# Optimization experiments

Hardware: AMD Instinct MI355X
Metric: run time of the kernel (lower is better)

Reference implementation:

```python
import jax, jax.numpy as jnp
import numpy as np

B, S, E, H = 1, 2048, 512, 8
D = E // H
N = B * S
WIN_HALF = 32  # attention_window 64 -> +/-32
ALPHA = 0.1
LN_EPS = 1e-12
NEG_INF = -1e9


def _build_window_edges():
    # windowed graph: dst i attends to src j with |i-j| <= WIN_HALF, within each batch block
    i = np.arange(S)
    offs = np.arange(-WIN_HALF, WIN_HALF + 1)
    src = i[:, None] + offs[None, :]
    dst = np.broadcast_to(i[:, None], src.shape)
    valid = (src >= 0) & (src < S)
    src, dst = src[valid], dst[valid]
    srcs, dsts = [], []
    for b in range(B):
        srcs.append(src + b * S)
        dsts.append(dst + b * S)
    return (np.concatenate(srcs).astype(np.int32),
            np.concatenate(dsts).astype(np.int32))


def setup_inputs() -> dict:
    key = jax.random.key(0)
    ks = jax.random.split(key, 12)
    sc = 1.0 / np.sqrt(E)
    src_np, dst_np = _build_window_edges()
    return {
        "hidden_states": jax.random.normal(ks[0], (B, S, E), dtype=jnp.float32),
        "attention_mask": jnp.zeros((B, S), dtype=jnp.float32),
        "edge_src": jnp.asarray(src_np),
        "edge_dst": jnp.asarray(dst_np),
        "Wq": jax.random.normal(ks[1], (E, E), dtype=jnp.float32) * sc,
        "bq": jnp.zeros((E,), dtype=jnp.float32),
        "Wk": jax.random.normal(ks[2], (E, E), dtype=jnp.float32) * sc,
        "bk": jnp.zeros((E,), dtype=jnp.float32),
        "Wv": jax.random.normal(ks[3], (E, E), dtype=jnp.float32) * sc,
        "bv": jnp.zeros((E,), dtype=jnp.float32),
        "Wo": jax.random.normal(ks[4], (E, E), dtype=jnp.float32) * sc,
        "bo": jnp.zeros((E,), dtype=jnp.float32),
        "ln_g": jnp.ones((E,), dtype=jnp.float32),
        "ln_b": jnp.zeros((E,), dtype=jnp.float32),
    }


def reference(hidden_states, attention_mask, edge_src, edge_dst,
              Wq, bq, Wk, bk, Wv, bv, Wo, bo, ln_g, ln_b):
    x = hidden_states  # (B,S,E); node ordering n = b*S + s (matches torch reshape)
    q = ((x @ Wq + bq) / jnp.sqrt(jnp.asarray(D, x.dtype))).reshape(N, H, D)
    k = (x @ Wk + bk).reshape(N, H, D)
    v = (x @ Wv + bv).reshape(N, H, D)

    mask = (attention_mask >= 0).reshape(N)  # bool per node

    # u_dot_v('k','q','score'): per-edge, per-head dot product
    score = jnp.einsum('ehd,ehd->eh', k[edge_src], q[edge_dst])  # (Eg,H)
    score = jnp.where(mask[edge_src][:, None], score, NEG_INF)

    # edge_softmax over incoming edges of each destination node
    smax = jax.ops.segment_max(score, edge_dst, num_segments=N)
    p = jnp.exp(score - smax[edge_dst])
    denom = jax.ops.segment_sum(p, edge_dst, num_segments=N)
    p = p / denom[edge_dst]  # (Eg,H)

    # 5 diffusion steps: h <- A h, blended with residual v (dropout off in eval)
    h = v
    for _ in range(5):
        m = h[edge_src] * p[:, :, None]                      # u_mul_e
        h = jax.ops.segment_sum(m, edge_dst, num_segments=N)  # sum('m','h')
        h = (1.0 - ALPHA) * h + ALPHA * v

    attn = h.reshape(B, S, E)

    # DiffuserSelfOutput: dense -> residual add -> LayerNorm
    y = attn @ Wo + bo + hidden_states
    mu = y.mean(-1, keepdims=True)
    var = ((y - mu) ** 2).mean(-1, keepdims=True)
    out = (y - mu) * jax.lax.rsqrt(var + LN_EPS) * ln_g + ln_b
    return out
```

## Files before the change

kernel.cpp:

```cpp
#include <hip/hip_runtime.h>
#include <math.h>

#define S_LEN 2048
#define E_DIM 512
#define NE (S_LEN * E_DIM)
#define H_NUM 8
#define WH 32
#define NOFF 65
#define PROW (H_NUM * NOFF)
#define PN (S_LEN * PROW)

typedef float f32x4 __attribute__((ext_vector_type(4)));
typedef short short8 __attribute__((ext_vector_type(8)));

__device__ __forceinline__ unsigned short f2bf(float f) {
    union { float f; unsigned u; } cv; cv.f = f;
    unsigned u = cv.u;
    u += 0x7fffu + ((u >> 16) & 1u);
    return (unsigned short)(u >> 16);
}
__device__ __forceinline__ unsigned pk2(float x, float y) {
    return (unsigned)f2bf(x) | ((unsigned)f2bf(y) << 16);
}

#define LGKM_BARRIER() do {                                   \
    __builtin_amdgcn_sched_barrier(0);                        \
    asm volatile("s_waitcnt lgkmcnt(0)" ::: "memory");        \
    __builtin_amdgcn_s_barrier();                             \
    __builtin_amdgcn_sched_barrier(0);                        \
} while (0)

__device__ __forceinline__ void mfma_gemm_f32(
    const float* __restrict__ A, const float* __restrict__ W,
    const float* __restrict__ bias, float* __restrict__ C,
    float scale, int m0, int n0)
{
    __shared__ unsigned short As[2][64 * 40];
    __shared__ unsigned short Bs[2][64 * 40];
    const int tid = threadIdx.x;
    const int lane = tid & 63, wave = tid >> 6;
    const int quad = lane >> 4, l16 = lane & 15;
    const int wr = (wave >> 1) * 32, wc = (wave & 1) * 32;
    const int ar = tid >> 2, ac = (tid & 3) * 8;
    const int bn = tid & 63, bk0 = (tid >> 6) * 8;

    f32x4 acc00 = {0.f,0.f,0.f,0.f}, acc01 = acc00, acc10 = acc00, acc11 = acc00;

    const float* Arow = A + (size_t)(m0 + ar) * E_DIM;

    float4 a0r[2], a1r[2];
    float  br[2][8];

#define QLOAD(s_, i_) do {                                                    \
        int kk_ = (i_) * 32;                                                  \
        a0r[s_] = *(const float4*)(Arow + kk_ + ac);                          \
        a1r[s_] = *(const float4*)(Arow + kk_ + ac + 4);                      \
        _Pragma("unroll")                                                     \
        for (int j_ = 0; j_ < 8; ++j_)                                        \
            br[s_][j_] = W[(size_t)(kk_ + bk0 + j_) * E_DIM + n0 + bn];       \
    } while (0)

#define QPACK(s_, b_) do {                                                    \
        uint4 ap_;                                                            \
        ap_.x = pk2(a0r[s_].x, a0r[s_].y); ap_.y = pk2(a0r[s_].z, a0r[s_].w); \
        ap_.z = pk2(a1r[s_].x, a1r[s_].y); ap_.w = pk2(a1r[s_].z, a1r[s_].w); \
        *(uint4*)(&As[b_][0] + ar * 40 + ac) = ap_;                           \
        uint4 bp_;                                                            \
        bp_.x = pk2(br[s_][0], br[s_][1]); bp_.y = pk2(br[s_][2], br[s_][3]); \
        bp_.z = pk2(br[s_][4], br[s_][5]); bp_.w = pk2(br[s_][6], br[s_][7]); \
        *(uint4*)(&Bs[b_][0] + bn * 40 + bk0) = bp_;                          \
    } while (0)

    QLOAD(0, 0);
    QPACK(0, 0);
    QLOAD(1, 1);
    LGKM_BARRIER();

#pragma unroll
    for (int it = 0; it < 16; ++it) {
        if (it < 14) QLOAD(it & 1, it + 2);

        const unsigned short* Ab = &As[it & 1][0];
        const unsigned short* Bb = &Bs[it & 1][0];
        short8 fa0 = *(const short8*)(Ab + (wr + l16) * 40 + quad * 8);
        short8 fa1 = *(const short8*)(Ab + (wr + 16 + l16) * 40 + quad * 8);
        short8 fb0 = *(const short8*)(Bb + (wc + l16) * 40 + quad * 8);
        short8 fb1 = *(const short8*)(Bb + (wc + 16 + l16) * 40 + quad * 8);
        acc00 = __builtin_amdgcn_mfma_f32_16x16x32_bf16(fa0, fb0, acc00, 0, 0, 0);
        acc01 = __builtin_amdgcn_mfma_f32_16x16x32_bf16(fa0, fb1, acc01, 0, 0, 0);
        acc10 = __builtin_amdgcn_mfma_f32_16x16x32_bf16(fa1, fb0, acc10, 0, 0, 0);
        acc11 = __builtin_amdgcn_mfma_f32_16x16x32_bf16(fa1, fb1, acc11, 0, 0, 0);

        if (it < 15) {
            QPACK((it + 1) & 1, (it + 1) & 1);
            LGKM_BARRIER();
        }
    }
#undef QLOAD
#undef QPACK

#pragma unroll
    for (int mi = 0; mi < 2; ++mi) {
#pragma unroll
        for (int ni = 0; ni < 2; ++ni) {
            f32x4 a = (mi == 0) ? ((ni == 0) ? acc00 : acc01)
                                : ((ni == 0) ? acc10 : acc11);
            int n = n0 + wc + ni * 16 + l16;
            float bval = bias[n];
#pragma unroll
            for (int r = 0; r < 4; ++r) {
                int m = m0 + wr + mi * 16 + quad * 4 + r;
                C[(size_t)m * E_DIM + n] = (a[r] + bval) * scale;
            }
        }
    }
}

__global__ __launch_bounds__(256)
void qkv_gemm(const float* __restrict__ x,
              const float* __restrict__ Wq, const float* __restrict__ bq,
              const float* __restrict__ Wk, const float* __restrict__ bk,
              const float* __restrict__ Wv, const float* __restrict__ bv,
              float* __restrict__ q, float* __restrict__ k, float* __restrict__ v)
{
    const float* W; const float* b; float* o; float sc;
    if (blockIdx.z == 0)      { W = Wq; b = bq; o = q; sc = 0.125f; }
    else if (blockIdx.z == 1) { W = Wk; b = bk; o = k; sc = 1.0f; }
    else                      { W = Wv; b = bv; o = v; sc = 1.0f; }
    mfma_gemm_f32(x, W, b, o, sc, blockIdx.y * 64, blockIdx.x * 64);
}

#define SDN 32
__global__ __launch_bounds__(256)
void scores_d1(const float* __restrict__ q, const float* __restrict__ k,
               const float* __restrict__ v, const float* __restrict__ amask,
               float* __restrict__ P, float* __restrict__ hA)
{
    const int i0 = blockIdx.x * SDN;
    const int h  = blockIdx.y;
    const int tid = threadIdx.x;
    __shared__ float ks[96 * 68];
    __shared__ float am[96];
    __shared__ float ps[SDN * NOFF];

    for (int e = tid; e < 96 * 16; e += 256) {
        int lr = e >> 4, c4 = e & 15;
        int j = i0 - WH + lr;
        int jc = min(max(j, 0), S_LEN - 1);
        *(float4*)(ks + lr * 68 + c4 * 4) =
            *(const float4*)(k + (size_t)jc * E_DIM + h * 64 + c4 * 4);
    }
    if (tid < 96) {
        int j = i0 - WH + tid;
        am[tid] = (j >= 0 && j < S_LEN) ? amask[j] : -1.0f;
    }

    const int dst = tid >> 3;
    const int og  = tid & 7;
    float4 qreg[16];
    {
        const float4* qrow = (const float4*)(q + (size_t)(i0 + dst) * E_DIM + h * 64);
#pragma unroll
        for (int t = 0; t < 16; ++t) qreg[t] = qrow[t];
    }
    __syncthreads();

    float sreg[9];
#pragma unroll
    for (int t = 0; t < 9; ++t) sreg[t] = -INFINITY;
#pragma unroll
    for (int t = 0; t < 9; ++t) {
        int off = og + 8 * t;
        if (off > 64) break;
        int j = i0 + dst + off - WH;
        if (j >= 0 && j < S_LEN) {
            int lr = dst + off;
            const float4* kr = (const float4*)(ks + lr * 68);
            float acc = 0.f;
#pragma unroll
            for (int u = 0; u < 16; ++u) {
                float4 a = qreg[u], bb = kr[u];
                acc += a.x * bb.x + a.y * bb.y + a.z * bb.z + a.w * bb.w;
            }
            sreg[t] = (am[lr] >= 0.f) ? acc : -1e9f;
        }
    }
    __syncthreads();

    for (int e = tid; e < 96 * 16; e += 256) {
        int lr = e >> 4, c4 = e & 15;
        int j = i0 - WH + lr;
        int jc = min(max(j, 0), S_LEN - 1);
        *(float4*)(ks + lr * 68 + c4 * 4) =
            *(const float4*)(v + (size_t)jc * E_DIM + h * 64 + c4 * 4);
    }

    float mx = sreg[0];
#pragma unroll
    for (int t = 1; t < 9; ++t) mx = fmaxf(mx, sreg[t]);
#pragma unroll
    for (int o = 1; o < 8; o <<= 1) mx = fmaxf(mx, __shfl_xor(mx, o, 64));
    float dn = 0.f;
#pragma unroll
    for (int t = 0; t < 9; ++t) {
        sreg[t] = expf(sreg[t] - mx);
        dn += sreg[t];
    }
#pragma unroll
    for (int o = 1; o < 8; o <<= 1) dn += __shfl_xor(dn, o, 64);
    float rinv = 1.f / dn;
#pragma unroll
    for (int t = 0; t < 9; ++t) {
        int off = og + 8 * t;
        if (off > 64) break;
        float pv = sreg[t] * rinv;
        P[(size_t)(i0 + dst) * PROW + h * NOFF + off] = pv;
        ps[dst * NOFF + off] = pv;
    }
    __syncthreads();

    {
        const int ci = tid & 15;
        const int ob = (tid >> 4) * 2;
        float4 a0 = {0,0,0,0}, a1 = a0;
        for (int lr = ob; lr < ob + 66; ++lr) {
            float4 hval = *(const float4*)(ks + lr * 68 + ci * 4);
            int o0 = lr - ob;
            if (o0 <= 64) {
                float p = ps[ob * NOFF + o0];
                a0.x += p * hval.x; a0.y += p * hval.y; a0.z += p * hval.z; a0.w += p * hval.w;
            }
            int o1 = o0 - 1;
            if ((unsigned)o1 <= 64u) {
                float p = ps[(ob + 1) * NOFF + o1];
                a1.x += p * hval.x; a1.y += p * hval.y; a1.z += p * hval.z; a1.w += p * hval.w;
            }
        }
#pragma unroll
        for (int r = 0; r < 2; ++r) {
            float4 a = r ? a1 : a0;
            float4 vv = *(const float4*)(ks + (WH + ob + r) * 68 + ci * 4);
            float4 o;
            o.x = 0.9f * a.x + 0.1f * vv.x;
            o.y = 0.9f * a.y + 0.1f * vv.y;
            o.z = 0.9f * a.z + 0.1f * vv.z;
            o.w = 0.9f * a.w + 0.1f * vv.w;
            *(float4*)(hA + (size_t)(i0 + ob + r) * E_DIM + h * 64 + ci * 4) = o;
        }
    }
}

__global__ __launch_bounds__(512)
void diffuse3m(const float* __restrict__ hin, const float* __restrict__ v,
               const float* __restrict__ P, float* __restrict__ hout)
{
    __shared__ unsigned short inT[64 * 264];
    __shared__ unsigned short m1T[64 * 200];
    __shared__ unsigned short ps[192 * 66];
    unsigned short* m2T = inT;
    const int i0 = blockIdx.x * 64;
    const int h  = blockIdx.y;
    const int c0 = h * 64;
    const int tid  = threadIdx.x;
    const int lane = tid & 63, wave = tid >> 6;
    const int quad = lane >> 4, l16 = lane & 15;

    for (int e = tid; e < 128 * 16; e += 512) {
        int rp = (e >> 4) * 2, c4 = (e & 15) * 4;
        int ja = min(max(i0 - 96 + rp,     0), S_LEN - 1);
        int jb = min(max(i0 - 96 + rp + 1, 0), S_LEN - 1);
        float4 ha = *(const float4*)(hin + (size_t)ja * E_DIM + c0 + c4);
        float4 hb = *(const float4*)(hin + (size_t)jb * E_DIM + c0 + c4);
        *(unsigned*)(inT + (c4 + 0) * 264 + rp) = pk2(ha.x, hb.x);
        *(unsigned*)(inT + (c4 + 1) * 264 + rp) = pk2(ha.y, hb.y);
        *(unsigned*)(inT + (c4 + 2) * 264 + rp) = pk2(ha.z, hb.z);
        *(unsigned*)(inT + (c4 + 3) * 264 + rp) = pk2(ha.w, hb.w);
    }
    for (int e = tid; e < 192 * 33; e += 512) {
        int mr = e / 33, t = e - mr * 33;
        int jc = min(max(i0 - 64 + mr, 0), S_LEN - 1);
        const float* pr = P + (size_t)jc * PROW + h * NOFF;
        if (t < 32)
            *(unsigned*)(ps + mr * 66 + t * 2) = pk2(pr[t * 2], pr[t * 2 + 1]);
        else
            ps[mr * 66 + 64] = f2bf(pr[64]);
    }
    __syncthreads();

#pragma unroll
    for (int uu = 0; uu < 3; ++uu) {
        int u = wave + uu * 8;
        int mtb = (u >> 1) * 16;
        int ntb = (u & 1) * 32;
        f32x4 a0 = {0.f,0.f,0.f,0.f}, a1 = a0;
        int ks0 = mtb >> 5;
        const int m = mtb + l16;
#pragma unroll
        for (int t = 0; t < 3; ++t) {
            int k0q = (ks0 + t) * 32 + quad * 8;
            short8 fa;
#pragma unroll
            for (int j = 0; j < 8; ++j) {
                int idx = k0q + j - m;
                int idc = min(max(idx, 0), 64);
                unsigned short pv = ps[m * 66 + idc];
                fa[j] = ((unsigned)idx <= 64u) ? (short)pv : (short)0;
            }
            short8 fb0 = *(const short8*)(inT + (ntb + l16) * 264 + k0q);
            short8 fb1 = *(const short8*)(inT + (ntb + 16 + l16) * 264 + k0q);
            a0 = __builtin_amdgcn_mfma_f32_16x16x32_bf16(fa, fb0, a0, 0, 0, 0);
            a1 = __builtin_amdgcn_mfma_f32_16x16x32_bf16(fa, fb1, a1, 0, 0, 0);
        }
#pragma unroll
        for (int nt = 0; nt < 2; ++nt) {
            f32x4 a = nt ? a1 : a0;
            int n = ntb + nt * 16 + l16;
            float o[4];
#pragma unroll
            for (int r = 0; r < 4; ++r) {
                int gm = min(max(i0 - 64 + mtb + quad * 4 + r, 0), S_LEN - 1);
                o[r] = 0.9f * a[r] + 0.1f * v[(size_t)gm * E_DIM + c0 + n];
            }
            *(unsigned*)(m1T + n * 200 + mtb + quad * 4)     = pk2(o[0], o[1]);
            *(unsigned*)(m1T + n * 200 + mtb + quad * 4 + 2) = pk2(o[2], o[3]);
        }
    }
    __syncthreads();

#pragma unroll
    for (int uu = 0; uu < 2; ++uu) {
        int u = wave + uu * 8;
        int mtb = (u >> 1) * 16;
        int ntb = (u & 1) * 32;
        f32x4 a0 = {0.f,0.f,0.f,0.f}, a1 = a0;
        int ks0 = mtb >> 5;
        const int m = mtb + l16;
#pragma unroll
        for (int t = 0; t < 3; ++t) {
            int k0q = (ks0 + t) * 32 + quad * 8;
            short8 fa;
#pragma unroll
            for (int j = 0; j < 8; ++j) {
                int idx = k0q + j - m;
                int idc = min(max(idx, 0), 64);
                unsigned short pv = ps[(m + 32) * 66 + idc];
                fa[j] = ((unsigned)idx <= 64u) ? (short)pv : (short)0;
            }
            short8 fb0 = *(const short8*)(m1T + (ntb + l16) * 200 + k0q);
            short8 fb1 = *(const short8*)(m1T + (ntb + 16 + l16) * 200 + k0q);
            a0 = __builtin_amdgcn_mfma_f32_16x16x32_bf16(fa, fb0, a0, 0, 0, 0);
            a1 = __builtin_amdgcn_mfma_f32_16x16x32_bf16(fa, fb1, a1, 0, 0, 0);
        }
        __syncthreads();
#pragma unroll
        for (int nt = 0; nt < 2; ++nt) {
            f32x4 a = nt ? a1 : a0;
            int n = ntb + nt * 16 + l16;
            float o[4];
#pragma unroll
            for (int r = 0; r < 4; ++r) {
                int gm = min(max(i0 - 32 + mtb + quad * 4 + r, 0), S_LEN - 1);
                o[r] = 0.9f * a[r] + 0.1f * v[(size_t)gm * E_DIM + c0 + n];
            }
            *(unsigned*)(m2T + n * 136 + mtb + quad * 4)     = pk2(o[0], o[1]);
            *(unsigned*)(m2T + n * 136 + mtb + quad * 4 + 2) = pk2(o[2], o[3]);
        }
    }
    __syncthreads();

    {
        int u = wave;
        int mtb = (u >> 1) * 16;
        int ntb = (u & 1) * 32;
        f32x4 a0 = {0.f,0.f,0.f,0.f}, a1 = a0;
        int ks0 = mtb >> 5;
        const int m = mtb + l16;
#pragma unroll
        for (int t = 0; t < 3; ++t) {
            int k0q = (ks0 + t) * 32 + quad * 8;
            short8 fa;
#pragma unroll
            for (int j = 0; j < 8; ++j) {
                int idx = k0q + j - m;
                int idc = min(max(idx, 0), 64);
                unsigned short pv = ps[(m + 64) * 66 + idc];
                fa[j] = ((unsigned)idx <= 64u) ? (short)pv : (short)0;
            }
            short8 fb0 = *(const short8*)(m2T + (ntb + l16) * 136 + k0q);
            short8 fb1 = *(const short8*)(m2T + (ntb + 16 + l16) * 136 + k0q);
            a0 = __builtin_amdgcn_mfma_f32_16x16x32_bf16(fa, fb0, a0, 0, 0, 0);
            a1 = __builtin_amdgcn_mfma_f32_16x16x32_bf16(fa, fb1, a1, 0, 0, 0);
        }
#pragma unroll
        for (int nt = 0; nt < 2; ++nt) {
            f32x4 a = nt ? a1 : a0;
            int n = ntb + nt * 16 + l16;
#pragma unroll
            for (int r = 0; r < 4; ++r) {
                int gm = i0 + mtb + quad * 4 + r;
                size_t base = (size_t)gm * E_DIM + c0 + n;
                hout[base] = 0.9f * a[r] + 0.1f * v[base];
            }
        }
    }
}

__global__ __launch_bounds__(512)
void oln4(const float* __restrict__ h4, const float* __restrict__ v,
          const float* __restrict__ P, const float* __restrict__ Wo,
          const float* __restrict__ bo, const float* __restrict__ x,
          const float* __restrict__ g, const float* __restrict__ lb,
          float* __restrict__ out)
{
    __shared__ unsigned short As16[16 * 520];
    __shared__ unsigned short Bs2[2][512 * 40];
    __shared__ float rsum[8][16], rsq[8][16];
    unsigned short* h4T  = &Bs2[0][0];
    unsigned short* ps16 = &Bs2[0][0] + 26624;

    const int tid = threadIdx.x;
    const int lane = tid & 63, wave = tid >> 6;
    const int quad = lane >> 4, l16 = lane & 15;
    const int m0 = blockIdx.x * 16;
    const int n = tid;

    for (int e = tid; e < 16 * 260; e += 512) {
        int mr = e / 260, t = e - mr * 260;
        const float* pr = P + (size_t)(m0 + mr) * PROW;
        *(unsigned*)(ps16 + mr * 528 + t * 2) = pk2(pr[t * 2], pr[t * 2 + 1]);
    }

    for (int hc = 0; hc < 2; ++hc) {
        for (int e = tid; e < 64 * 64; e += 512) {
            int r = e & 63, c4 = (e >> 6) * 4;
            int row = min(max(m0 - 32 + r, 0), S_LEN - 1);
            float4 hv = *(const float4*)(h4 + (size_t)row * E_DIM + hc * 256 + c4);
            h4T[(c4 + 0) * 104 + r] = f2bf(hv.x);
            h4T[(c4 + 1) * 104 + r] = f2bf(hv.y);
            h4T[(c4 + 2) * 104 + r] = f2bf(hv.z);
            h4T[(c4 + 3) * 104 + r] = f2bf(hv.w);
        }
        for (int e = tid; e < 32 * 64; e += 512) {
            int r = 64 + (e & 31), c4 = (e >> 5) * 4;
            int row = min(max(m0 - 32 + r, 0), S_LEN - 1);
            float4 hv = *(const float4*)(h4 + (size_t)row * E_DIM + hc * 256 + c4);
            h4T[(c4 + 0) * 104 + r] = f2bf(hv.x);
            h4T[(c4 + 1) * 104 + r] = f2bf(hv.y);
            h4T[(c4 + 2) * 104 + r] = f2bf(hv.z);
            h4T[(c4 + 3) * 104 + r] = f2bf(hv.w);
        }
        __syncthreads();

        {
            const int hd = hc * 4 + (wave >> 1);
            short8 fa[3];
#pragma unroll
            for (int t = 0; t < 3; ++t) {
                int k0q = t * 32 + quad * 8;
#pragma unroll
                for (int j = 0; j < 8; ++j) {
                    int idx = k0q + j - l16;
                    int idc = min(max(idx, 0), 64);
                    unsigned short pv = ps16[l16 * 528 + hd * NOFF + idc];
                    fa[t][j] = ((unsigned)idx <= 64u) ? (short)pv : (short)0;
                }
            }
#pragma unroll
            for (int nt = 0; nt < 2; ++nt) {
                int lc = wave * 32 + nt * 16;
                f32x4 ba = {0.f, 0.f, 0.f, 0.f};
#pragma unroll
                for (int t = 0; t < 3; ++t) {
                    short8 fb = *(const short8*)(h4T + (lc + l16) * 104 + t * 32 + quad * 8);
                    ba = __builtin_amdgcn_mfma_f32_16x16x32_bf16(fa[t], fb, ba, 0, 0, 0);
                }
                int gcol = hc * 256 + lc + l16;
#pragma unroll
                for (int r = 0; r < 4; ++r) {
                    int m = quad * 4 + r;
                    float vv = v[(size_t)(m0 + m) * E_DIM + gcol];
                    As16[m * 520 + gcol] = f2bf(0.9f * ba[r] + 0.1f * vv);
                }
            }
        }
        __syncthreads();
    }

    {
        float w0[32];
#pragma unroll
        for (int j = 0; j < 32; ++j)
            w0[j] = Wo[(size_t)j * E_DIM + n];
#pragma unroll
        for (int t = 0; t < 4; ++t) {
            uint4 bp;
            bp.x = pk2(w0[t*8+0], w0[t*8+1]); bp.y = pk2(w0[t*8+2], w0[t*8+3]);
            bp.z = pk2(w0[t*8+4], w0[t*8+5]); bp.w = pk2(w0[t*8+6], w0[t*8+7]);
            *(uint4*)(&Bs2[0][0] + n * 40 + t * 8) = bp;
        }
    }
    LGKM_BARRIER();

    f32x4 acc[4];
#pragma unroll
    for (int t = 0; t < 4; ++t) acc[t] = (f32x4){0.f,0.f,0.f,0.f};

#pragma unroll
    for (int it = 0; it < 16; ++it) {
        float wn[32];
        if (it < 15) {
#pragma unroll
            for (int j = 0; j < 32; ++j)
                wn[j] = Wo[(size_t)((it + 1) * 32 + j) * E_DIM + n];
        }

        short8 fa = *(const short8*)(As16 + l16 * 520 + it * 32 + quad * 8);
#pragma unroll
        for (int nt = 0; nt < 4; ++nt) {
            short8 fb = *(const short8*)(&Bs2[it & 1][0] +
                                         (wave * 64 + nt * 16 + l16) * 40 + quad * 8);
            acc[nt] = __builtin_amdgcn_mfma_f32_16x16x32_bf16(fa, fb, acc[nt], 0, 0, 0);
        }

        if (it < 15) {
#pragma unroll
            for (int t = 0; t < 4; ++t) {
                uint4 bp;
                bp.x = pk2(wn[t*8+0], wn[t*8+1]); bp.y = pk2(wn[t*8+2], wn[t*8+3]);
                bp.z = pk2(wn[t*8+4], wn[t*8+5]); bp.w = pk2(wn[t*8+6], wn[t*8+7]);
                *(uint4*)(&Bs2[(it + 1) & 1][0] + n * 40 + t * 8) = bp;
            }
            LGKM_BARRIER();
        }
    }

    float s[4] = {0.f,0.f,0.f,0.f}, s2[4] = {0.f,0.f,0.f,0.f};
#pragma unroll
    for (int nt = 0; nt < 4; ++nt) {
        int nc = wave * 64 + nt * 16 + l16;
        float bv = bo[nc];
#pragma unroll
        for (int r = 0; r < 4; ++r) {
            int m = m0 + quad * 4 + r;
            float vl = acc[nt][r] + bv + x[(size_t)m * E_DIM + nc];
            acc[nt][r] = vl;
            s[r] += vl; s2[r] += vl * vl;
        }
    }
#pragma unroll
    for (int o = 1; o < 16; o <<= 1) {
#pragma unroll
        for (int r = 0; r < 4; ++r) {
            s[r]  += __shfl_xor(s[r], o, 64);
            s2[r] += __shfl_xor(s2[r], o, 64);
        }
    }
    if (l16 == 0) {
#pragma unroll
        for (int r = 0; r < 4; ++r) {
            rsum[wave][quad * 4 + r] = s[r];
            rsq[wave][quad * 4 + r]  = s2[r];
        }
    }
    __syncthreads();
    float mu[4], rs[4];
#pragma unroll
    for (int r = 0; r < 4; ++r) {
        int rl = quad * 4 + r;
        float tot = 0.f, tot2 = 0.f;
#pragma unroll
        for (int w = 0; w < 8; ++w) { tot += rsum[w][rl]; tot2 += rsq[w][rl]; }
        float m_ = tot * (1.f / 512.f);
        float var = tot2 * (1.f / 512.f) - m_ * m_;
        mu[r] = m_; rs[r] = rsqrtf(var + 1e-12f);
    }
#pragma unroll
    for (int nt = 0; nt < 4; ++nt) {
        int nc = wave * 64 + nt * 16 + l16;
        float gv = g[nc], bbv = lb[nc];
#pragma unroll
        for (int r = 0; r < 4; ++r) {
            int m = m0 + quad * 4 + r;
            out[(size_t)m * E_DIM + nc] = (acc[nt][r] - mu[r]) * rs[r] * gv + bbv;
        }
    }
}

extern "C" void kernel_launch(void* const* d_in, const int* in_sizes, int n_in,
                              void* d_out, int out_size, void* d_ws, size_t ws_size,
                              hipStream_t stream)
{
    const float* x     = (const float*)d_in[0];
    const float* amask = (const float*)d_in[1];
    const float* Wq = (const float*)d_in[4];
    const float* bq = (const float*)d_in[5];
    const float* Wk = (const float*)d_in[6];
    const float* bk = (const float*)d_in[7];
    const float* Wv = (const float*)d_in[8];
    const float* bv = (const float*)d_in[9];
    const float* Wo = (const float*)d_in[10];
    const float* bo = (const float*)d_in[11];
    const float* lng = (const float*)d_in[12];
    const float* lnb = (const float*)d_in[13];
    float* out = (float*)d_out;

    float* ws = (float*)d_ws;
    float* q  = ws;
    float* k  = ws + (size_t)NE;
    float* v  = ws + (size_t)2 * NE;
    float* P  = ws + (size_t)3 * NE;
    float* hA = ws + (size_t)3 * NE + PN;
    float* hB = hA + (size_t)NE;

    qkv_gemm<<<dim3(8, 32, 3), 256, 0, stream>>>(x, Wq, bq, Wk, bk, Wv, bv, q, k, v);

    scores_d1<<<dim3(64, 8), 256, 0, stream>>>(q, k, v, amask, P, hA);

    diffuse3m<<<dim3(32, 8), 512, 0, stream>>>(hA, v, P, hB);

    oln4<<<128, 512, 0, stream>>>(hB, v, P, Wo, bo, x, lng, lnb, out);
}
```

Baseline: 165.3 us.

## Move fifth diffusion step into diffuse kernel and pass bf16 result to output GEMM

New measurement: 164.4 us. About the same (-0.6%).

```diff
diff --git a/kernel.cpp b/kernel.cpp
--- a/kernel.cpp
+++ b/kernel.cpp
@@ -251,13 +251,14 @@
 }
 
 __global__ __launch_bounds__(512)
-void diffuse3m(const float* __restrict__ hin, const float* __restrict__ v,
-               const float* __restrict__ P, float* __restrict__ hout)
+void diffuse4m(const float* __restrict__ hin, const float* __restrict__ v,
+               const float* __restrict__ P, unsigned short* __restrict__ h5b)
 {
-    __shared__ unsigned short inT[64 * 264];
-    __shared__ unsigned short m1T[64 * 200];
-    __shared__ unsigned short ps[192 * 66];
+    __shared__ unsigned short inT[64 * 328];
+    __shared__ unsigned short m1T[64 * 264];
+    __shared__ unsigned short ps[256 * 66];
     unsigned short* m2T = inT;
+    unsigned short* m3T = m1T;
     const int i0 = blockIdx.x * 64;
     const int h  = blockIdx.y;
     const int c0 = h * 64;
@@ -265,25 +266,65 @@
     const int lane = tid & 63, wave = tid >> 6;
     const int quad = lane >> 4, l16 = lane & 15;
 
-    for (int e = tid; e < 128 * 16; e += 512) {
+    for (int e = tid; e < 160 * 16; e += 512) {
         int rp = (e >> 4) * 2, c4 = (e & 15) * 4;
-        int ja = min(max(i0 - 96 + rp,     0), S_LEN - 1);
-        int jb = min(max(i0 - 96 + rp + 1, 0), S_LEN - 1);
+        int ja = min(max(i0 - 128 + rp,     0), S_LEN - 1);
+        int jb = min(max(i0 - 128 + rp + 1, 0), S_LEN - 1);
         float4 ha = *(const float4*)(hin + (size_t)ja * E_DIM + c0 + c4);
         float4 hb = *(const float4*)(hin + (size_t)jb * E_DIM + c0 + c4);
-        *(unsigned*)(inT + (c4 + 0) * 264 + rp) = pk2(ha.x, hb.x);
-        *(unsigned*)(inT + (c4 + 1) * 264 + rp) = pk2(ha.y, hb.y);
-        *(unsigned*)(inT + (c4 + 2) * 264 + rp) = pk2(ha.z, hb.z);
-        *(unsigned*)(inT + (c4 + 3) * 264 + rp) = pk2(ha.w, hb.w);
-    }
-    for (int e = tid; e < 192 * 33; e += 512) {
+        *(unsigned*)(inT + (c4 + 0) * 328 + rp) = pk2(ha.x, hb.x);
+        *(unsigned*)(inT + (c4 + 1) * 328 + rp) = pk2(ha.y, hb.y);
+        *(unsigned*)(inT + (c4 + 2) * 328 + rp) = pk2(ha.z, hb.z);
+        *(unsigned*)(inT + (c4 + 3) * 328 + rp) = pk2(ha.w, hb.w);
+    }
+    for (int e = tid; e < 256 * 33; e += 512) {
         int mr = e / 33, t = e - mr * 33;
-        int jc = min(max(i0 - 64 + mr, 0), S_LEN - 1);
+        int jc = min(max(i0 - 96 + mr, 0), S_LEN - 1);
         const float* pr = P + (size_t)jc * PROW + h * NOFF;
         if (t < 32)
             *(unsigned*)(ps + mr * 66 + t * 2) = pk2(pr[t * 2], pr[t * 2 + 1]);
         else
             ps[mr * 66 + 64] = f2bf(pr[64]);
+    }
+    __syncthreads();
+
+#pragma unroll
+    for (int uu = 0; uu < 4; ++uu) {
+        int u = wave + uu * 8;
+        int mtb = (u >> 1) * 16;
+        int ntb = (u & 1) * 32;
+        f32x4 a0 = {0.f,0.f,0.f,0.f}, a1 = a0;
+        int ks0 = mtb >> 5;
+        const int m = mtb + l16;
+#pragma unroll
+        for (int t = 0; t < 3; ++t) {
+            int k0q = (ks0 + t) * 32 + quad * 8;
+            short8 fa;
+#pragma unroll
+            for (int j = 0; j < 8; ++j) {
+                int idx = k0q + j - m;
+                int idc = min(max(idx, 0), 64);
+                unsigned short pv = ps[m * 66 + idc];
+                fa[j] = ((unsigned)idx <= 64u) ? (short)pv : (short)0;
+            }
+            short8 fb0 = *(const short8*)(inT + (ntb + l16) * 328 + k0q);
+            short8 fb1 = *(const short8*)(inT + (ntb + 16 + l16) * 328 + k0q);
+            a0 = __builtin_amdgcn_mfma_f32_16x16x32_bf16(fa, fb0, a0, 0, 0, 0);
+            a1 = __builtin_amdgcn_mfma_f32_16x16x32_bf16(fa, fb1, a1, 0, 0, 0);
+        }
+#pragma unroll
+        for (int nt = 0; nt < 2; ++nt) {
+            f32x4 a = nt ? a1 : a0;
+            int n = ntb + nt * 16 + l16;
+            float o[4];
+#pragma unroll
+            for (int r = 0; r < 4; ++r) {
+                int gm = min(max(i0 - 96 + mtb + quad * 4 + r, 0), S_LEN - 1);
+                o[r] = 0.9f * a[r] + 0.1f * v[(size_t)gm * E_DIM + c0 + n];
+            }
+            *(unsigned*)(m1T + n * 264 + mtb + quad * 4)     = pk2(o[0], o[1]);
+            *(unsigned*)(m1T + n * 264 + mtb + quad * 4 + 2) = pk2(o[2], o[3]);
+        }
     }
     __syncthreads();
 
@@ -303,11 +344,11 @@
             for (int j = 0; j < 8; ++j) {
                 int idx = k0q + j - m;
                 int idc = min(max(idx, 0), 64);
-                unsigned short pv = ps[m * 66 + idc];
+                unsigned short pv = ps[(m + 32) * 66 + idc];
                 fa[j] = ((unsigned)idx <= 64u) ? (short)pv : (short)0;
             }
-            short8 fb0 = *(const short8*)(inT + (ntb + l16) * 264 + k0q);
-            short8 fb1 = *(const short8*)(inT + (ntb + 16 + l16) * 264 + k0q);
+            short8 fb0 = *(const short8*)(m1T + (ntb + l16) * 264 + k0q);
+            short8 fb1 = *(const short8*)(m1T + (ntb + 16 + l16) * 264 + k0q);
             a0 = __builtin_amdgcn_mfma_f32_16x16x32_bf16(fa, fb0, a0, 0, 0, 0);
             a1 = __builtin_amdgcn_mfma_f32_16x16x32_bf16(fa, fb1, a1, 0, 0, 0);
         }
@@ -321,8 +362,8 @@
                 int gm = min(max(i0 - 64 + mtb + quad * 4 + r, 0), S_LEN - 1);
                 o[r] = 0.9f * a[r] + 0.1f * v[(size_t)gm * E_DIM + c0 + n];
             }
-            *(unsigned*)(m1T + n * 200 + mtb + quad * 4)     = pk2(o[0], o[1]);
-            *(unsigned*)(m1T + n * 200 + mtb + quad * 4 + 2) = pk2(o[2], o[3]);
+            *(unsigned*)(m2T + n * 200 + mtb + quad * 4)     = pk2(o[0], o[1]);
+            *(unsigned*)(m2T + n * 200 + mtb + quad * 4 + 2) = pk2(o[2], o[3]);
         }
     }
     __syncthreads();
@@ -343,15 +384,14 @@
             for (int j = 0; j < 8; ++j) {
                 int idx = k0q + j - m;
                 int idc = min(max(idx, 0), 64);
-                unsigned short pv = ps[(m + 32) * 66 + idc];
+                unsigned short pv = ps[(m + 64) * 66 + idc];
                 fa[j] = ((unsigned)idx <= 64u) ? (short)pv : (short)0;
             }
-            short8 fb0 = *(const short8*)(m1T + (ntb + l16) * 200 + k0q);
-            short8 fb1 = *(const short8*)(m1T + (ntb + 16 + l16) * 200 + k0q);
+            short8 fb0 = *(const short8*)(m2T + (ntb + l16) * 200 + k0q);
+            short8 fb1 = *(const short8*)(m2T + (ntb + 16 + l16) * 200 + k0q);
             a0 = __builtin_amdgcn_mfma_f32_16x16x32_bf16(fa, fb0, a0, 0, 0, 0);
             a1 = __builtin_amdgcn_mfma_f32_16x16x32_bf16(fa, fb1, a1, 0, 0, 0);
         }
-        __syncthreads();
 #pragma unroll
         for (int nt = 0; nt < 2; ++nt) {
             f32x4 a = nt ? a1 : a0;
@@ -362,8 +402,8 @@
                 int gm = min(max(i0 - 32 + mtb + quad * 4 + r, 0), S_LEN - 1);
                 o[r] = 0.9f * a[r] + 0.1f * v[(size_t)gm * E_DIM + c0 + n];
             }
-            *(unsigned*)(m2T + n * 136 + mtb + quad * 4)     = pk2(o[0], o[1]);
-            *(unsigned*)(m2T + n * 136 + mtb + quad * 4 + 2) = pk2(o[2], o[3]);
+            *(unsigned*)(m3T + n * 136 + mtb + quad * 4)     = pk2(o[0], o[1]);
+            *(unsigned*)(m3T + n * 136 + mtb + quad * 4 + 2) = pk2(o[2], o[3]);
         }
     }
     __syncthreads();
@@ -383,11 +423,11 @@
             for (int j = 0; j < 8; ++j) {
                 int idx = k0q + j - m;
                 int idc = min(max(idx, 0), 64);
-                unsigned short pv = ps[(m + 64) * 66 + idc];
+                unsigned short pv = ps[(m + 96) * 66 + idc];
                 fa[j] = ((unsigned)idx <= 64u) ? (short)pv : (short)0;
             }
-            short8 fb0 = *(const short8*)(m2T + (ntb + l16) * 136 + k0q);
-            short8 fb1 = *(const short8*)(m2T + (ntb + 16 + l16) * 136 + k0q);
+            short8 fb0 = *(const short8*)(m3T + (ntb + l16) * 136 + k0q);
+            short8 fb1 = *(const short8*)(m3T + (ntb + 16 + l16) * 136 + k0q);
             a0 = __builtin_amdgcn_mfma_f32_16x16x32_bf16(fa, fb0, a0, 0, 0, 0);
             a1 = __builtin_amdgcn_mfma_f32_16x16x32_bf16(fa, fb1, a1, 0, 0, 0);
         }
@@ -398,93 +438,31 @@
 #pragma unroll
             for (int r = 0; r < 4; ++r) {
                 int gm = i0 + mtb + quad * 4 + r;
-                size_t base = (size_t)gm * E_DIM + c0 + n;
-                hout[base] = 0.9f * a[r] + 0.1f * v[base];
+                float vv = v[(size_t)gm * E_DIM + c0 + n];
+                h5b[(size_t)gm * E_DIM + c0 + n] = f2bf(0.9f * a[r] + 0.1f * vv);
             }
         }
     }
 }
 
 __global__ __launch_bounds__(512)
-void oln4(const float* __restrict__ h4, const float* __restrict__ v,
-          const float* __restrict__ P, const float* __restrict__ Wo,
+void oln5(const unsigned short* __restrict__ h5b, const float* __restrict__ Wo,
           const float* __restrict__ bo, const float* __restrict__ x,
           const float* __restrict__ g, const float* __restrict__ lb,
           float* __restrict__ out)
 {
-    __shared__ unsigned short As16[16 * 520];
     __shared__ unsigned short Bs2[2][512 * 40];
     __shared__ float rsum[8][16], rsq[8][16];
-    unsigned short* h4T  = &Bs2[0][0];
-    unsigned short* ps16 = &Bs2[0][0] + 26624;
-
     const int tid = threadIdx.x;
     const int lane = tid & 63, wave = tid >> 6;
     const int quad = lane >> 4, l16 = lane & 15;
     const int m0 = blockIdx.x * 16;
     const int n = tid;
 
-    for (int e = tid; e < 16 * 260; e += 512) {
-        int mr = e / 260, t = e - mr * 260;
-        const float* pr = P + (size_t)(m0 + mr) * PROW;
-        *(unsigned*)(ps16 + mr * 528 + t * 2) = pk2(pr[t * 2], pr[t * 2 + 1]);
-    }
-
-    for (int hc = 0; hc < 2; ++hc) {
-        for (int e = tid; e < 64 * 64; e += 512) {
-            int r = e & 63, c4 = (e >> 6) * 4;
-            int row = min(max(m0 - 32 + r, 0), S_LEN - 1);
-            float4 hv = *(const float4*)(h4 + (size_t)row * E_DIM + hc * 256 + c4);
-            h4T[(c4 + 0) * 104 + r] = f2bf(hv.x);
-            h4T[(c4 + 1) * 104 + r] = f2bf(hv.y);
-            h4T[(c4 + 2) * 104 + r] = f2bf(hv.z);
-            h4T[(c4 + 3) * 104 + r] = f2bf(hv.w);
-        }
-        for (int e = tid; e < 32 * 64; e += 512) {
-            int r = 64 + (e & 31), c4 = (e >> 5) * 4;
-            int row = min(max(m0 - 32 + r, 0), S_LEN - 1);
-            float4 hv = *(const float4*)(h4 + (size_t)row * E_DIM + hc * 256 + c4);
-            h4T[(c4 + 0) * 104 + r] = f2bf(hv.x);
-            h4T[(c4 + 1) * 104 + r] = f2bf(hv.y);
-            h4T[(c4 + 2) * 104 + r] = f2bf(hv.z);
-            h4T[(c4 + 3) * 104 + r] = f2bf(hv.w);
-        }
-        __syncthreads();
-
-        {
-            const int hd = hc * 4 + (wave >> 1);
-            short8 fa[3];
-#pragma unroll
-            for (int t = 0; t < 3; ++t) {
-                int k0q = t * 32 + quad * 8;
-#pragma unroll
-                for (int j = 0; j < 8; ++j) {
-                    int idx = k0q + j - l16;
-                    int idc = min(max(idx, 0), 64);
-                    unsigned short pv = ps16[l16 * 528 + hd * NOFF + idc];
-                    fa[t][j] = ((unsigned)idx <= 64u) ? (short)pv : (short)0;
-                }
-            }
-#pragma unroll
-            for (int nt = 0; nt < 2; ++nt) {
-                int lc = wave * 32 + nt * 16;
-                f32x4 ba = {0.f, 0.f, 0.f, 0.f};
-#pragma unroll
-                for (int t = 0; t < 3; ++t) {
-                    short8 fb = *(const short8*)(h4T + (lc + l16) * 104 + t * 32 + quad * 8);
-                    ba = __builtin_amdgcn_mfma_f32_16x16x32_bf16(fa[t], fb, ba, 0, 0, 0);
-                }
-                int gcol = hc * 256 + lc + l16;
-#pragma unroll
-                for (int r = 0; r < 4; ++r) {
-                    int m = quad * 4 + r;
-                    float vv = v[(size_t)(m0 + m) * E_DIM + gcol];
-                    As16[m * 520 + gcol] = f2bf(0.9f * ba[r] + 0.1f * vv);
-                }
-            }
-        }
-        __syncthreads();
-    }
+    short8 far_[16];
+#pragma unroll
+    for (int t = 0; t < 16; ++t)
+        far_[t] = *(const short8*)(h5b + (size_t)(m0 + l16) * E_DIM + t * 32 + quad * 8);
 
     {
         float w0[32];
@@ -514,12 +492,11 @@
                 wn[j] = Wo[(size_t)((it + 1) * 32 + j) * E_DIM + n];
         }
 
-        short8 fa = *(const short8*)(As16 + l16 * 520 + it * 32 + quad * 8);
 #pragma unroll
         for (int nt = 0; nt < 4; ++nt) {
             short8 fb = *(const short8*)(&Bs2[it & 1][0] +
                                          (wave * 64 + nt * 16 + l16) * 40 + quad * 8);
-            acc[nt] = __builtin_amdgcn_mfma_f32_16x16x32_bf16(fa, fb, acc[nt], 0, 0, 0);
+            acc[nt] = __builtin_amdgcn_mfma_f32_16x16x32_bf16(far_[it], fb, acc[nt], 0, 0, 0);
         }
 
         if (it < 15) {
@@ -610,13 +587,13 @@
     float* v  = ws + (size_t)2 * NE;
     float* P  = ws + (size_t)3 * NE;
     float* hA = ws + (size_t)3 * NE + PN;
-    float* hB = hA + (size_t)NE;
+    unsigned short* h5b = (unsigned short*)(ws + (size_t)4 * NE + PN);
 
     qkv_gemm<<<dim3(8, 32, 3), 256, 0, stream>>>(x, Wq, bq, Wk, bk, Wv, bv, q, k, v);
 
     scores_d1<<<dim3(64, 8), 256, 0, stream>>>(q, k, v, amask, P, hA);
 
-    diffuse3m<<<dim3(32, 8), 512, 0, stream>>>(hA, v, P, hB);
-
-    oln4<<<128, 512, 0, stream>>>(hB, v, P, Wo, bo, x, lng, lnb, out);
-}
+    diffuse4m<<<dim3(32, 8), 512, 0, stream>>>(hA, v, P, h5b);
+
+    oln5<<<128, 512, 0, stream>>>(h5b, Wo, bo, x, lng, lnb, out);
+}
```
